# Optimization experiments

Hardware: AMD Instinct MI355X
Metric: run time of the kernel (lower is better)

The kernel has to match this reference:

```python
import jax, jax.numpy as jnp
import numpy as np

NEG_SLOPE = 0.2  # LeakyReLU(0.2) on the final Dense


def setup_inputs() -> dict:
    key = jax.random.key(0)
    k1, k2, k3, k4 = jax.random.split(key, 4)
    B, D = 256, 65536          # batch, input voxel dim
    N, G = 41, 2048            # n_groups, group size (overlapping allowed)
    O, E = 256, 512            # per-group output dim, embed_dim
    x = jax.random.normal(k1, (B, D), dtype=jnp.float32)
    group_idx = jax.random.randint(k2, (N, G), 0, D, dtype=jnp.int32)
    # He-normal-ish init for the per-group Dense weights
    W = jax.random.normal(k3, (N, G, O), dtype=jnp.float32) * np.float32(np.sqrt(2.0 / G))
    b = jnp.zeros((N, O), dtype=jnp.float32)
    W3 = jax.random.normal(k4, (N * O, E), dtype=jnp.float32) * np.float32(np.sqrt(2.0 / (N * O)))
    b3 = jnp.zeros((E,), dtype=jnp.float32)
    return {"x": x, "group_idx": group_idx, "W": W, "b": b, "W3": W3, "b3": b3}


def reference(x, group_idx, W, b, W3, b3):
    B = x.shape[0]
    # per-group gather: (B, N, G)
    g = x[:, group_idx]
    # N parallel Dense layers as one grouped GEMM: (B, N, O)
    h = jnp.einsum('bng,ngo->bno', g, W) + b
    # concat along feature axis -> (B, N*O); dropout is identity at inference
    h = h.reshape(B, -1)
    # final Dense + LeakyReLU(0.2)
    out = h @ W3 + b3
    return jnp.where(out >= 0, out, NEG_SLOPE * out)
```

## Files before the change

### kernel.cpp

```cpp
#include <hip/hip_runtime.h>
#include <hip/hip_bf16.h>

#define NB 256
#define DD 65536
#define NN 41
#define GG 2048
#define OO 256
#define NO 10496
#define EE 512
#define NEG_SLOPE 0.2f

typedef __attribute__((ext_vector_type(8))) short bf16x8;
typedef __attribute__((ext_vector_type(4))) float f32x4;
typedef unsigned int u32;

__device__ __forceinline__ void gl_lds16(const __hip_bfloat16* gsrc, __hip_bfloat16* lds) {
    __builtin_amdgcn_global_load_lds((const __attribute__((address_space(1))) u32*)gsrc,
                                     (__attribute__((address_space(3))) u32*)lds, 16, 0, 0);
}

__device__ __forceinline__ u32 pack_bf2(float lo, float hi) {
    u32 a = (u32)__bfloat16_as_ushort(__float2bfloat16(lo));
    u32 b = (u32)__bfloat16_as_ushort(__float2bfloat16(hi));
    return a | (b << 16);
}

__global__ __launch_bounds__(256) void transpose_w3_k(const float* __restrict__ W3,
                                                      __hip_bfloat16* __restrict__ W3t) {
    __shared__ u32 tb[64 * 128];
    int rem = blockIdx.x;
    int kc0 = (rem >> 3) * 256;
    int o0 = (rem & 7) * 64;
    const int K = NO, Oc = EE;
    int t = threadIdx.x;
    int p = t & 127;
    int oh = (t >> 7) * 32;
    const float* r0 = W3 + (size_t)(kc0 + 2 * p) * Oc + o0 + oh;
    const float* r1 = r0 + Oc;
#pragma unroll
    for (int c = 0; c < 8; ++c) {
        float4 a = *(const float4*)&r0[c * 4];
        float4 b = *(const float4*)&r1[c * 4];
        tb[(oh + c * 4 + 0) * 128 + p] = pack_bf2(a.x, b.x);
        tb[(oh + c * 4 + 1) * 128 + p] = pack_bf2(a.y, b.y);
        tb[(oh + c * 4 + 2) * 128 + p] = pack_bf2(a.z, b.z);
        tb[(oh + c * 4 + 3) * 128 + p] = pack_bf2(a.w, b.w);
    }
    __syncthreads();
    int w = t >> 6, l = t & 63;
    int lr = l >> 5;
    int ls = l & 31;
#pragma unroll
    for (int j = 0; j < 8; ++j) {
        int o = j * 8 + w * 2 + lr;
        uint4 v = *(const uint4*)&tb[o * 128 + ls * 4];
        *(uint4*)&W3t[(size_t)(o0 + o) * K + kc0 + ls * 8] = v;
    }
}

__global__ __launch_bounds__(1024) void gather_full_k(const float* __restrict__ x,
                                                      const int* __restrict__ idx,
                                                      __hip_bfloat16* __restrict__ g) {
    extern __shared__ __hip_bfloat16 xr[];
    int b = blockIdx.x;
    int t = threadIdx.x;
    const float4* xv = (const float4*)(x + (size_t)b * DD);
#pragma unroll
    for (int i = 0; i < 16; ++i) {
        float4 v = xv[t + 1024 * i];
        short4 p;
        p.x = (short)__bfloat16_as_ushort(__float2bfloat16(v.x));
        p.y = (short)__bfloat16_as_ushort(__float2bfloat16(v.y));
        p.z = (short)__bfloat16_as_ushort(__float2bfloat16(v.z));
        p.w = (short)__bfloat16_as_ushort(__float2bfloat16(v.w));
        *(short4*)&xr[(t + 1024 * i) * 4] = p;
    }
    __syncthreads();
    const int4* idx4 = (const int4*)idx;
    for (int u = t; u < NN * GG / 4; u += 1024) {
        int4 ii = idx4[u];
        int n = u >> 9;
        int k = (u & 511) * 4;
        ushort4 o;
        o.x = __bfloat16_as_ushort(xr[ii.x]);
        o.y = __bfloat16_as_ushort(xr[ii.y]);
        o.z = __bfloat16_as_ushort(xr[ii.z]);
        o.w = __bfloat16_as_ushort(xr[ii.w]);
        *(ushort4*)&g[((size_t)n * NB + b) * GG + k] = o;
    }
}

__global__ __launch_bounds__(512) void gather_half_k(const float* __restrict__ x,
                                                     const int* __restrict__ idx,
                                                     __hip_bfloat16* __restrict__ g) {
    __shared__ __align__(16) __hip_bfloat16 xr[32768];
    int b = blockIdx.x >> 1;
    int h = blockIdx.x & 1;
    int t = threadIdx.x;
    const float4* xv = (const float4*)(x + (size_t)b * DD + h * 32768);
#pragma unroll
    for (int i = 0; i < 16; ++i) {
        float4 v = xv[t + 512 * i];
        short4 p;
        p.x = (short)__bfloat16_as_ushort(__float2bfloat16(v.x));
        p.y = (short)__bfloat16_as_ushort(__float2bfloat16(v.y));
        p.z = (short)__bfloat16_as_ushort(__float2bfloat16(v.z));
        p.w = (short)__bfloat16_as_ushort(__float2bfloat16(v.w));
        *(short4*)&xr[(t + 512 * i) * 4] = p;
    }
    __syncthreads();
    const int4* idx4 = (const int4*)idx;
    for (int u = t; u < NN * GG / 4; u += 512) {
        int4 ii = idx4[u];
        int n = u >> 9;
        int k = (u & 511) * 4;
        __hip_bfloat16* dst = &g[((size_t)n * NB + b) * GG + k];
        if ((ii.x >> 15) == h) dst[0] = xr[ii.x & 32767];
        if ((ii.y >> 15) == h) dst[1] = xr[ii.y & 32767];
        if ((ii.z >> 15) == h) dst[2] = xr[ii.z & 32767];
        if ((ii.w >> 15) == h) dst[3] = xr[ii.w & 32767];
    }
}

__global__ __launch_bounds__(256) void gemm1_k(const __hip_bfloat16* __restrict__ g,
                                               const float* __restrict__ W,
                                               __hip_bfloat16* __restrict__ part1) {
    int bid0 = blockIdx.x;
    int bid = (bid0 & 7) * 82 + (bid0 >> 3);
    int s = bid & 3;
    int o0 = ((bid >> 2) & 1) * 128;
    int m0 = ((bid >> 3) & 1) * 128;
    int n = bid >> 4;
    const __hip_bfloat16* srcA = g + ((size_t)n * NB + m0) * GG + s * 512;
    const float* srcB = W + ((size_t)n * GG + s * 512) * OO + o0;
    __shared__ __align__(16) __hip_bfloat16 lA[2][128 * 32];
    __shared__ __align__(16) __hip_bfloat16 lB[2][128 * 32];
    int t = threadIdx.x;
    int lane = t & 63, w = t >> 6;
    int mw = (w >> 1) * 64, ow = (w & 1) * 64;
    int lrow = lane & 15, quad = lane >> 4;
    int r0 = t >> 2, q0 = (t & 3) * 8;
    int bp = t >> 4;
    int boq = t & 15;
    int bswz = (boq & 3) << 2;
    const float* wb0 = srcB + (size_t)(2 * bp) * OO + boq * 8;
    f32x4 acc[4][4] = {};

    {
        float4 a0 = *(const float4*)&wb0[0];
        float4 a1 = *(const float4*)&wb0[4];
        float4 b0 = *(const float4*)&wb0[OO];
        float4 b1 = *(const float4*)&wb0[OO + 4];
        u32* d = (u32*)&lB[0][0];
        int ob = boq * 8;
        int pw = bp ^ bswz;
        d[(ob + 0) * 16 + pw] = pack_bf2(a0.x, b0.x);
        d[(ob + 1) * 16 + pw] = pack_bf2(a0.y, b0.y);
        d[(ob + 2) * 16 + pw] = pack_bf2(a0.z, b0.z);
        d[(ob + 3) * 16 + pw] = pack_bf2(a0.w, b0.w);
        d[(ob + 4) * 16 + pw] = pack_bf2(a1.x, b1.x);
        d[(ob + 5) * 16 + pw] = pack_bf2(a1.y, b1.y);
        d[(ob + 6) * 16 + pw] = pack_bf2(a1.z, b1.z);
        d[(ob + 7) * 16 + pw] = pack_bf2(a1.w, b1.w);
    }
    gl_lds16(srcA + (size_t)r0 * GG + q0, &lA[0][t * 8]);
    gl_lds16(srcA + (size_t)(r0 + 64) * GG + q0, &lA[0][(t + 256) * 8]);
    __syncthreads();
#pragma unroll 1
    for (int it = 0; it < 16; ++it) {
        int cur = it & 1;
        float4 a0, a1, b0, b1;
        bool pf = (it + 1 < 16);
        if (pf) {
            int k1 = (it + 1) * 32;
            const float* wn = wb0 + (size_t)k1 * OO;
            a0 = *(const float4*)&wn[0];
            a1 = *(const float4*)&wn[4];
            b0 = *(const float4*)&wn[OO];
            b1 = *(const float4*)&wn[OO + 4];
            gl_lds16(srcA + (size_t)r0 * GG + k1 + q0, &lA[1 - cur][t * 8]);
            gl_lds16(srcA + (size_t)(r0 + 64) * GG + k1 + q0, &lA[1 - cur][(t + 256) * 8]);
        }
        bf16x8 af[4];
#pragma unroll
        for (int fm = 0; fm < 4; ++fm)
            af[fm] = *(const bf16x8*)&lA[cur][(mw + fm * 16 + lrow) * 32 + quad * 8];
        const u32* lbu = (const u32*)&lB[cur][0];
#pragma unroll
        for (int fn = 0; fn < 4; ++fn) {
            int orow = ow + fn * 16 + lrow;
            int fsw = ((orow >> 3) & 3) << 2;
            bf16x8 bfr = *(const bf16x8*)&lbu[orow * 16 + (quad * 4 ^ fsw)];
#pragma unroll
            for (int fm = 0; fm < 4; ++fm)
                acc[fm][fn] = __builtin_amdgcn_mfma_f32_16x16x32_bf16(af[fm], bfr, acc[fm][fn], 0, 0, 0);
        }
        if (pf) {
            u32* d = (u32*)&lB[1 - cur][0];
            int ob = boq * 8;
            int pw = bp ^ bswz;
            d[(ob + 0) * 16 + pw] = pack_bf2(a0.x, b0.x);
            d[(ob + 1) * 16 + pw] = pack_bf2(a0.y, b0.y);
            d[(ob + 2) * 16 + pw] = pack_bf2(a0.z, b0.z);
            d[(ob + 3) * 16 + pw] = pack_bf2(a0.w, b0.w);
            d[(ob + 4) * 16 + pw] = pack_bf2(a1.x, b1.x);
            d[(ob + 5) * 16 + pw] = pack_bf2(a1.y, b1.y);
            d[(ob + 6) * 16 + pw] = pack_bf2(a1.z, b1.z);
            d[(ob + 7) * 16 + pw] = pack_bf2(a1.w, b1.w);
        }
        __syncthreads();
    }
#pragma unroll
    for (int fm = 0; fm < 4; ++fm) {
#pragma unroll
        for (int fn = 0; fn < 4; ++fn) {
            int col = o0 + ow + fn * 16 + lrow;
#pragma unroll
            for (int r = 0; r < 4; ++r) {
                int row = m0 + mw + fm * 16 + quad * 4 + r;
                part1[((size_t)s * NB + row) * NO + n * OO + col] = __float2bfloat16(acc[fm][fn][r]);
            }
        }
    }
}

__global__ __launch_bounds__(256) void combine1_k(const __hip_bfloat16* __restrict__ part1,
                                                  const float* __restrict__ bias,
                                                  __hip_bfloat16* __restrict__ h) {
    int j4 = blockIdx.x * 256 + threadIdx.x;
    int jj = j4 % (NO / 4);
    float4 a = ((const float4*)bias)[jj];
#pragma unroll
    for (int s = 0; s < 4; ++s) {
        ushort4 p = *(const ushort4*)&part1[(size_t)s * NB * NO + (size_t)j4 * 4];
        a.x += __bfloat162float(__ushort_as_bfloat16(p.x));
        a.y += __bfloat162float(__ushort_as_bfloat16(p.y));
        a.z += __bfloat162float(__ushort_as_bfloat16(p.z));
        a.w += __bfloat162float(__ushort_as_bfloat16(p.w));
    }
    ushort4 o;
    o.x = __bfloat16_as_ushort(__float2bfloat16(a.x));
    o.y = __bfloat16_as_ushort(__float2bfloat16(a.y));
    o.z = __bfloat16_as_ushort(__float2bfloat16(a.z));
    o.w = __bfloat16_as_ushort(__float2bfloat16(a.w));
    *(ushort4*)&h[(size_t)j4 * 4] = o;
}

__global__ __launch_bounds__(256) void gemm2_k(const __hip_bfloat16* __restrict__ h,
                                               const __hip_bfloat16* __restrict__ W3t,
                                               float* __restrict__ part) {
    int bid0 = blockIdx.x;
    int bid = (bid0 & 7) * 82 + (bid0 >> 3);
    int e0 = (bid & 7) * 64;
    int m0 = ((bid >> 3) & 1) * 128;
    int s = bid >> 4;
    const __hip_bfloat16* srcA = h + (size_t)m0 * NO + s * 256;
    const __hip_bfloat16* srcB = W3t + (size_t)e0 * NO + s * 256;
    __shared__ __align__(16) __hip_bfloat16 lA[2][128 * 32];
    __shared__ __align__(16) __hip_bfloat16 lB[2][64 * 32];
    int t = threadIdx.x;
    int lane = t & 63, w = t >> 6;
    int mw = (w >> 1) * 64, ew = (w & 1) * 32;
    int lrow = lane & 15, quad = lane >> 4;
    int rA = t >> 2, qA = (t & 3) * 8;
    int rB = t >> 2, qB = (t & 3) * 8;
    f32x4 acc[4][2] = {};

    gl_lds16(srcA + (size_t)rA * NO + qA, &lA[0][t * 8]);
    gl_lds16(srcA + (size_t)(rA + 64) * NO + qA, &lA[0][(t + 256) * 8]);
    gl_lds16(srcB + (size_t)(rB & 63) * NO + qB, &lB[0][t * 8]);
    __syncthreads();
#pragma unroll 1
    for (int it = 0; it < 8; ++it) {
        int cur = it & 1;
        if (it + 1 < 8) {
            int k1 = (it + 1) * 32;
            gl_lds16(srcA + (size_t)rA * NO + k1 + qA, &lA[1 - cur][t * 8]);
            gl_lds16(srcA + (size_t)(rA + 64) * NO + k1 + qA, &lA[1 - cur][(t + 256) * 8]);
            gl_lds16(srcB + (size_t)(rB & 63) * NO + k1 + qB, &lB[1 - cur][t * 8]);
        }
        bf16x8 af[4];
#pragma unroll
        for (int fm = 0; fm < 4; ++fm)
            af[fm] = *(const bf16x8*)&lA[cur][(mw + fm * 16 + lrow) * 32 + quad * 8];
#pragma unroll
        for (int fn = 0; fn < 2; ++fn) {
            bf16x8 bfr = *(const bf16x8*)&lB[cur][(ew + fn * 16 + lrow) * 32 + quad * 8];
#pragma unroll
            for (int fm = 0; fm < 4; ++fm)
                acc[fm][fn] = __builtin_amdgcn_mfma_f32_16x16x32_bf16(af[fm], bfr, acc[fm][fn], 0, 0, 0);
        }
        __syncthreads();
    }
#pragma unroll
    for (int fm = 0; fm < 4; ++fm) {
#pragma unroll
        for (int fn = 0; fn < 2; ++fn) {
            int e = e0 + ew + fn * 16 + lrow;
#pragma unroll
            for (int r = 0; r < 4; ++r) {
                int row = m0 + mw + fm * 16 + quad * 4 + r;
                part[((size_t)s * NB + row) * EE + e] = acc[fm][fn][r];
            }
        }
    }
}

__global__ __launch_bounds__(128) void reduce_k(const float* __restrict__ part,
                                                const float* __restrict__ b3,
                                                float* __restrict__ out) {
    int j = blockIdx.x * 128 + threadIdx.x;
    float4 a = make_float4(0.f, 0.f, 0.f, 0.f);
    for (int s = 0; s < NN; ++s) {
        float4 v = ((const float4*)part)[(size_t)s * (NB * EE / 4) + j];
        a.x += v.x; a.y += v.y; a.z += v.z; a.w += v.w;
    }
    float4 bv = ((const float4*)b3)[j & 127];
    a.x += bv.x; a.y += bv.y; a.z += bv.z; a.w += bv.w;
    a.x = a.x >= 0.f ? a.x : NEG_SLOPE * a.x;
    a.y = a.y >= 0.f ? a.y : NEG_SLOPE * a.y;
    a.z = a.z >= 0.f ? a.z : NEG_SLOPE * a.z;
    a.w = a.w >= 0.f ? a.w : NEG_SLOPE * a.w;
    ((float4*)out)[j] = a;
}

extern "C" void kernel_launch(void* const* d_in, const int* in_sizes, int n_in,
                              void* d_out, int out_size, void* d_ws, size_t ws_size,
                              hipStream_t stream) {
    const float* x = (const float*)d_in[0];
    const int* idx = (const int*)d_in[1];
    const float* W = (const float*)d_in[2];
    const float* bias = (const float*)d_in[3];
    const float* W3 = (const float*)d_in[4];
    const float* b3 = (const float*)d_in[5];
    float* out = (float*)d_out;

    char* ws = (char*)d_ws;
    const size_t g_off = 0;
    const size_t g_sz = (size_t)NN * NB * GG * 2;
    const size_t wt_off = g_off + g_sz;
    const size_t wt_sz = (size_t)NN * GG * OO * 2;
    const size_t w3t_off = wt_off + wt_sz;
    const size_t w3t_sz = (size_t)NO * EE * 2;
    const size_t h_off = w3t_off + w3t_sz;
    const size_t h_sz = (size_t)NB * NO * 2;
    const size_t p_off = h_off + h_sz;

    __hip_bfloat16* g = (__hip_bfloat16*)(ws + g_off);
    __hip_bfloat16* W3t = (__hip_bfloat16*)(ws + w3t_off);
    __hip_bfloat16* h = (__hip_bfloat16*)(ws + h_off);
    __hip_bfloat16* part1 = (__hip_bfloat16*)(ws + p_off);
    float* part = (float*)(ws + p_off);

    transpose_w3_k<<<dim3(NN * 8), 256, 0, stream>>>(W3, W3t);
    hipError_t aerr = hipFuncSetAttribute(reinterpret_cast<const void*>(gather_full_k),
                                          hipFuncAttributeMaxDynamicSharedMemorySize, 131072);
    if (aerr == hipSuccess) {
        gather_full_k<<<dim3(NB), 1024, 131072, stream>>>(x, idx, g);
    } else {
        gather_half_k<<<dim3(512), 512, 0, stream>>>(x, idx, g);
    }
    gemm1_k<<<dim3(656), 256, 0, stream>>>(g, W, part1);
    combine1_k<<<dim3(NB * NO / 4 / 256), 256, 0, stream>>>(part1, bias, h);
    gemm2_k<<<dim3(656), 256, 0, stream>>>(h, W3t, part);
    reduce_k<<<dim3(256), 128, 0, stream>>>(part, b3, out);
}
```

Baseline: 266.2 us.

## Enlarge gemm1 tile to full 256-row batch so W is loaded once per tile

The grouped GEMM now uses 512-thread blocks, each covering all 256 batch rows instead of 128. That halves the block count and means each W slice (fp32, converted to bf16 on the fly) is read and packed by only one block instead of two, cutting global W traffic. The LDS staging for A doubles and each thread handles half as many W elements. The partial-sum buffer is moved to the unused transposed-W workspace slot. The trade-off is fewer blocks (328) for the GPU's CUs and higher LDS use per block, which may reduce occupancy.

```diff
diff --git a/kernel.cpp b/kernel.cpp
--- a/kernel.cpp
+++ b/kernel.cpp
@@ -122,70 +122,61 @@
     }
 }
 
-__global__ __launch_bounds__(256) void gemm1_k(const __hip_bfloat16* __restrict__ g,
+__global__ __launch_bounds__(512) void gemm1_k(const __hip_bfloat16* __restrict__ g,
                                                const float* __restrict__ W,
                                                __hip_bfloat16* __restrict__ part1) {
     int bid0 = blockIdx.x;
-    int bid = (bid0 & 7) * 82 + (bid0 >> 3);
+    int bid = (bid0 & 7) * 41 + (bid0 >> 3);
     int s = bid & 3;
     int o0 = ((bid >> 2) & 1) * 128;
-    int m0 = ((bid >> 3) & 1) * 128;
-    int n = bid >> 4;
-    const __hip_bfloat16* srcA = g + ((size_t)n * NB + m0) * GG + s * 512;
+    int n = bid >> 3;
+    const __hip_bfloat16* srcA = g + (size_t)n * NB * GG + s * 512;
     const float* srcB = W + ((size_t)n * GG + s * 512) * OO + o0;
-    __shared__ __align__(16) __hip_bfloat16 lA[2][128 * 32];
-    __shared__ __align__(16) __hip_bfloat16 lB[2][128 * 32];
+    __shared__ __align__(16) __hip_bfloat16 lA[2][256 * 32];
+    __shared__ __align__(16) u32 lB[2][128 * 16];
     int t = threadIdx.x;
     int lane = t & 63, w = t >> 6;
     int mw = (w >> 1) * 64, ow = (w & 1) * 64;
     int lrow = lane & 15, quad = lane >> 4;
     int r0 = t >> 2, q0 = (t & 3) * 8;
-    int bp = t >> 4;
-    int boq = t & 15;
-    int bswz = (boq & 3) << 2;
-    const float* wb0 = srcB + (size_t)(2 * bp) * OO + boq * 8;
+    int bp = (t >> 4) & 15;
+    int boq8 = t & 15;
+    int hi = w >> 2;
+    int cb = boq8 * 8 + hi * 4;
+    int pw = bp ^ ((boq8 & 3) << 2);
+    const float* wb0 = srcB + (size_t)(2 * bp) * OO + cb;
     f32x4 acc[4][4] = {};
 
     {
         float4 a0 = *(const float4*)&wb0[0];
-        float4 a1 = *(const float4*)&wb0[4];
         float4 b0 = *(const float4*)&wb0[OO];
-        float4 b1 = *(const float4*)&wb0[OO + 4];
-        u32* d = (u32*)&lB[0][0];
-        int ob = boq * 8;
-        int pw = bp ^ bswz;
-        d[(ob + 0) * 16 + pw] = pack_bf2(a0.x, b0.x);
-        d[(ob + 1) * 16 + pw] = pack_bf2(a0.y, b0.y);
-        d[(ob + 2) * 16 + pw] = pack_bf2(a0.z, b0.z);
-        d[(ob + 3) * 16 + pw] = pack_bf2(a0.w, b0.w);
-        d[(ob + 4) * 16 + pw] = pack_bf2(a1.x, b1.x);
-        d[(ob + 5) * 16 + pw] = pack_bf2(a1.y, b1.y);
-        d[(ob + 6) * 16 + pw] = pack_bf2(a1.z, b1.z);
-        d[(ob + 7) * 16 + pw] = pack_bf2(a1.w, b1.w);
+        u32* d = &lB[0][0];
+        d[(cb + 0) * 16 + pw] = pack_bf2(a0.x, b0.x);
+        d[(cb + 1) * 16 + pw] = pack_bf2(a0.y, b0.y);
+        d[(cb + 2) * 16 + pw] = pack_bf2(a0.z, b0.z);
+        d[(cb + 3) * 16 + pw] = pack_bf2(a0.w, b0.w);
     }
     gl_lds16(srcA + (size_t)r0 * GG + q0, &lA[0][t * 8]);
-    gl_lds16(srcA + (size_t)(r0 + 64) * GG + q0, &lA[0][(t + 256) * 8]);
+    gl_lds16(srcA + (size_t)(r0 + 128) * GG + q0, &lA[0][(t + 512) * 8]);
     __syncthreads();
 #pragma unroll 1
     for (int it = 0; it < 16; ++it) {
         int cur = it & 1;
-        float4 a0, a1, b0, b1;
+        float4 a0, b0;
         bool pf = (it + 1 < 16);
         if (pf) {
             int k1 = (it + 1) * 32;
             const float* wn = wb0 + (size_t)k1 * OO;
             a0 = *(const float4*)&wn[0];
-            a1 = *(const float4*)&wn[4];
             b0 = *(const float4*)&wn[OO];
-            b1 = *(const float4*)&wn[OO + 4];
             gl_lds16(srcA + (size_t)r0 * GG + k1 + q0, &lA[1 - cur][t * 8]);
-            gl_lds16(srcA + (size_t)(r0 + 64) * GG + k1 + q0, &lA[1 - cur][(t + 256) * 8]);
+            gl_lds16(srcA + (size_t)(r0 + 128) * GG + k1 + q0, &lA[1 - cur][(t + 512) * 8]);
         }
         bf16x8 af[4];
 #pragma unroll
         for (int fm = 0; fm < 4; ++fm)
             af[fm] = *(const bf16x8*)&lA[cur][(mw + fm * 16 + lrow) * 32 + quad * 8];
-        const u32* lbu = (const u32*)&lB[cur][0];
+        const u32* lbu = &lB[cur][0];
 #pragma unroll
         for (int fn = 0; fn < 4; ++fn) {
             int orow = ow + fn * 16 + lrow;
@@ -196,17 +187,11 @@
                 acc[fm][fn] = __builtin_amdgcn_mfma_f32_16x16x32_bf16(af[fm], bfr, acc[fm][fn], 0, 0, 0);
         }
         if (pf) {
-            u32* d = (u32*)&lB[1 - cur][0];
-            int ob = boq * 8;
-            int pw = bp ^ bswz;
-            d[(ob + 0) * 16 + pw] = pack_bf2(a0.x, b0.x);
-            d[(ob + 1) * 16 + pw] = pack_bf2(a0.y, b0.y);
-            d[(ob + 2) * 16 + pw] = pack_bf2(a0.z, b0.z);
-            d[(ob + 3) * 16 + pw] = pack_bf2(a0.w, b0.w);
-            d[(ob + 4) * 16 + pw] = pack_bf2(a1.x, b1.x);
-            d[(ob + 5) * 16 + pw] = pack_bf2(a1.y, b1.y);
-            d[(ob + 6) * 16 + pw] = pack_bf2(a1.z, b1.z);
-            d[(ob + 7) * 16 + pw] = pack_bf2(a1.w, b1.w);
+            u32* d = &lB[1 - cur][0];
+            d[(cb + 0) * 16 + pw] = pack_bf2(a0.x, b0.x);
+            d[(cb + 1) * 16 + pw] = pack_bf2(a0.y, b0.y);
+            d[(cb + 2) * 16 + pw] = pack_bf2(a0.z, b0.z);
+            d[(cb + 3) * 16 + pw] = pack_bf2(a0.w, b0.w);
         }
         __syncthreads();
     }
@@ -217,7 +202,7 @@
             int col = o0 + ow + fn * 16 + lrow;
 #pragma unroll
             for (int r = 0; r < 4; ++r) {
-                int row = m0 + mw + fm * 16 + quad * 4 + r;
+                int row = mw + fm * 16 + quad * 4 + r;
                 part1[((size_t)s * NB + row) * NO + n * OO + col] = __float2bfloat16(acc[fm][fn][r]);
             }
         }
@@ -349,7 +334,7 @@
     __hip_bfloat16* g = (__hip_bfloat16*)(ws + g_off);
     __hip_bfloat16* W3t = (__hip_bfloat16*)(ws + w3t_off);
     __hip_bfloat16* h = (__hip_bfloat16*)(ws + h_off);
-    __hip_bfloat16* part1 = (__hip_bfloat16*)(ws + p_off);
+    __hip_bfloat16* part1 = (__hip_bfloat16*)(ws + wt_off);
     float* part = (float*)(ws + p_off);
 
     transpose_w3_k<<<dim3(NN * 8), 256, 0, stream>>>(W3, W3t);
@@ -360,7 +345,7 @@
     } else {
         gather_half_k<<<dim3(512), 512, 0, stream>>>(x, idx, g);
     }
-    gemm1_k<<<dim3(656), 256, 0, stream>>>(g, W, part1);
+    gemm1_k<<<dim3(328), 512, 0, stream>>>(g, W, part1);
     combine1_k<<<dim3(NB * NO / 4 / 256), 256, 0, stream>>>(part1, bias, h);
     gemm2_k<<<dim3(656), 256, 0, stream>>>(h, W3t, part);
     reduce_k<<<dim3(256), 128, 0, stream>>>(part, b3, out);
```

Result: no change. 261.2 us (-1.9%).
